# Kernel tuning notes

Hardware: AMD Instinct MI355X
Metric: run time of the kernel (lower is better)

## Reference

```python
import jax, jax.numpy as jnp
import numpy as np

MIN_SIZE = 16.0 / 800.0
PRE_NMS_TOP_K = 6000   # mode='test'
POST_NMS_TOP_K = 300   # mode='test'
IOU_THR = 0.7
H = W = 100
A = 9
N = H * W * A


def setup_inputs() -> dict:
    key = jax.random.key(0)
    k1, k2, k3 = jax.random.split(key, 3)
    pred_cls = jax.random.normal(k1, (1, H, W, 2 * A), dtype=jnp.float32)
    pred_reg = jax.random.normal(k2, (1, N, 4), dtype=jnp.float32) * 0.2
    # anchors as valid normalized xyxy boxes
    u = jax.random.uniform(k3, (N, 4), dtype=jnp.float32)
    cx = 0.05 + 0.9 * u[:, 0]
    cy = 0.05 + 0.9 * u[:, 1]
    w = 0.02 + 0.18 * u[:, 2]
    h = 0.02 + 0.18 * u[:, 3]
    anchor = jnp.stack([cx - w / 2, cy - h / 2, cx + w / 2, cy + h / 2], axis=1)
    return {"pred_cls": pred_cls, "pred_reg": pred_reg, "anchor": anchor}


def greedy_nms_mask(boxes, valid):
    # boxes: [K,4] sorted by descending score; valid: [K] bool
    K = boxes.shape[0]
    area = (boxes[:, 2] - boxes[:, 0]) * (boxes[:, 3] - boxes[:, 1])
    lt = jnp.maximum(boxes[:, None, :2], boxes[None, :, :2])   # [K,K,2]
    rb = jnp.minimum(boxes[:, None, 2:], boxes[None, :, 2:])
    wh = jnp.clip(rb - lt, 0.0)
    inter = wh[..., 0] * wh[..., 1]
    union = area[:, None] + area[None, :] - inter
    iou = inter / jnp.maximum(union, jnp.float32(1e-12))       # [K,K]
    idx = jnp.arange(K)

    def body(i, suppressed):
        keep_i = jnp.logical_not(suppressed[i]) & valid[i]
        return suppressed | (keep_i & (iou[i] > IOU_THR) & (idx > i))

    suppressed = jax.lax.fori_loop(0, K, body, jnp.zeros((K,), dtype=bool))
    return jnp.logical_not(suppressed) & valid


def reference(pred_cls, pred_reg, anchor):
    reg = pred_reg.reshape(-1, 4)                 # squeeze -> [N,4]
    # xy_to_cxcy(anchor)
    a_cxcy = jnp.concatenate([(anchor[:, 2:] + anchor[:, :2]) / 2,
                              anchor[:, 2:] - anchor[:, :2]], axis=1)
    # decode(reg, anchor_cxcy)
    cxcy = reg[:, :2] * a_cxcy[:, 2:] + a_cxcy[:, :2]
    wh = jnp.exp(reg[:, 2:]) * a_cxcy[:, 2:]
    # cxcy_to_xy(...).clamp(0,1)
    roi = jnp.clip(jnp.concatenate([cxcy - wh / 2, cxcy + wh / 2], axis=1), 0.0, 1.0)

    # objectness softmax over the 2-class logits
    probs = jax.nn.softmax(pred_cls.reshape(1, H, W, A, 2), axis=-1)[..., 1].reshape(-1)  # [N]

    # size filter
    ws = roi[:, 2] - roi[:, 0]
    hs = roi[:, 3] - roi[:, 1]
    size_ok = (hs >= MIN_SIZE) & (ws >= MIN_SIZE)
    masked_scores = jnp.where(size_ok, probs, -jnp.inf)

    # sort descending + take pre-NMS top-k (filtered boxes sort last)
    top_scores, top_idx = jax.lax.top_k(masked_scores, PRE_NMS_TOP_K)
    boxes = roi[top_idx]                           # [K,4]
    valid = size_ok[top_idx]

    kept = greedy_nms_mask(boxes, valid)           # [K] bool

    # first POST_NMS_TOP_K kept boxes in score order; pad with zeros
    rank = jnp.cumsum(kept.astype(jnp.int32)) - 1
    slot = jnp.where(kept & (rank < POST_NMS_TOP_K), rank, POST_NMS_TOP_K)
    out = jnp.zeros((POST_NMS_TOP_K, 4), dtype=boxes.dtype).at[slot].set(boxes, mode='drop')
    return out
```

## Files before the change

### kernel.cpp

```cpp
#include <hip/hip_runtime.h>
#include <stdint.h>

#pragma clang fp contract(off)

#define N_ANCH 90000
#define M_TOP  1024
#define M_L    512
#define NW_L   8
#define K_POST 300
#define CAP    2048
#define WINB   0x3D00
#define WINSZ  768
#define DB     32
#define MIN_SIZE (16.0f / 800.0f)
#define IOU_THR  0.7f

#define SIDX(j) ((j) + ((j) >> 6))
#define SB_SZ   (M_L + NW_L)

#define OFF_HISTB 0
#define OFF_CNT   98304
#define OFF_CAND  98368
#define OFF_ROI   114752
#define OFF_KEYS  1554752
#define OFF_SBOX  1914752
#define OFF_MASK  1931136

__global__ void __launch_bounds__(1024)
decode_score_kernel(const float2* __restrict__ cls,
                    const float4* __restrict__ reg,
                    const float4* __restrict__ anc,
                    float4* __restrict__ roi,
                    unsigned* __restrict__ keys,
                    int* __restrict__ histB) {
    __shared__ int lh[WINSZ];
    int tid = threadIdx.x;
    for (int k = tid; k < WINSZ; k += 1024) lh[k] = 0;
    __syncthreads();

    for (int n = blockIdx.x * 1024 + tid; n < N_ANCH; n += DB * 1024) {
        float4 a = anc[n];
        float4 r = reg[n];
        float aw  = a.z - a.x;
        float ah  = a.w - a.y;
        float acx = (a.z + a.x) * 0.5f;
        float acy = (a.w + a.y) * 0.5f;
        float cx = r.x * aw + acx;
        float cy = r.y * ah + acy;
        float w  = expf(r.z) * aw;
        float h  = expf(r.w) * ah;
        float x1 = fminf(fmaxf(cx - w * 0.5f, 0.0f), 1.0f);
        float y1 = fminf(fmaxf(cy - h * 0.5f, 0.0f), 1.0f);
        float x2 = fminf(fmaxf(cx + w * 0.5f, 0.0f), 1.0f);
        float y2 = fminf(fmaxf(cy + h * 0.5f, 0.0f), 1.0f);
        roi[n] = make_float4(x1, y1, x2, y2);

        float2 c = cls[n];
        float m  = fmaxf(c.x, c.y);
        float e0 = expf(c.x - m);
        float e1 = expf(c.y - m);
        float p  = e1 / (e0 + e1);

        bool ok = ((x2 - x1) >= MIN_SIZE) && ((y2 - y1) >= MIN_SIZE);
        unsigned key = ok ? (__float_as_uint(p) ^ 0x80000000u) : 0u;
        keys[n] = key;
        if (key != 0u) {
            int hb = (int)(key >> 16) - 0x8000;
            if (hb >= WINB) atomicAdd(&lh[hb - WINB], 1);
        }
    }
    __syncthreads();
    for (int k = tid; k < WINSZ; k += 1024)
        histB[blockIdx.x * WINSZ + k] = lh[k];
}

__global__ void __launch_bounds__(1024)
thrcompact_kernel(const unsigned* __restrict__ keys,
                  const int* __restrict__ histB,
                  int* __restrict__ cnt,
                  unsigned long long* __restrict__ cand) {
    __shared__ int rscan[1024];
    __shared__ int s_pos;
    __shared__ unsigned s_thr;
    int t = threadIdx.x;
    if (t == 0) s_pos = 0;
    int wsum = 0;
    if (t < WINSZ) {
        int bin = WINSZ - 1 - t;
#pragma unroll
        for (int b = 0; b < DB; ++b) wsum += histB[b * WINSZ + bin];
    }
    rscan[t] = wsum;
    __syncthreads();
    for (int off = 1; off < 1024; off <<= 1) {
        int add = (t >= off) ? rscan[t - off] : 0;
        __syncthreads();
        rscan[t] += add;
        __syncthreads();
    }
    if (t < WINSZ && rscan[t] >= M_TOP && (t == 0 || rscan[t - 1] < M_TOP))
        s_thr = ((unsigned)(0x8000 + WINB + (WINSZ - 1 - t))) << 16;
    if (t == 0 && rscan[WINSZ - 1] < M_TOP)
        s_thr = 0x80000000u;
    __syncthreads();
    unsigned thr = s_thr;
    const uint4* k4 = (const uint4*)keys;
    for (int g = t; g < N_ANCH / 4; g += 1024) {
        uint4 kv = k4[g];
        int n0 = g * 4;
        if (kv.x >= thr) { int p = atomicAdd(&s_pos, 1); if (p < CAP) cand[p] = ((unsigned long long)kv.x << 32) | (unsigned)(~(unsigned)n0); }
        if (kv.y >= thr) { int p = atomicAdd(&s_pos, 1); if (p < CAP) cand[p] = ((unsigned long long)kv.y << 32) | (unsigned)(~(unsigned)(n0 + 1)); }
        if (kv.z >= thr) { int p = atomicAdd(&s_pos, 1); if (p < CAP) cand[p] = ((unsigned long long)kv.z << 32) | (unsigned)(~(unsigned)(n0 + 2)); }
        if (kv.w >= thr) { int p = atomicAdd(&s_pos, 1); if (p < CAP) cand[p] = ((unsigned long long)kv.w << 32) | (unsigned)(~(unsigned)(n0 + 3)); }
    }
    __syncthreads();
    if (t == 0) cnt[0] = (s_pos < CAP) ? s_pos : CAP;
}

__global__ void __launch_bounds__(1024)
rank_select_kernel(const unsigned long long* __restrict__ cand,
                   const int* __restrict__ cnt,
                   const float4* __restrict__ roi,
                   float4* __restrict__ sbox) {
    __shared__ unsigned long long s[CAP];
    __shared__ int red[1024];
    int tid = threadIdx.x;
    int c = cnt[0];
    if (c > CAP) c = CAP;
    for (int k = tid; k < CAP; k += 1024) s[k] = (k < c) ? cand[k] : 0ULL;
    __syncthreads();
    int e = tid & 63;
    int slice = tid >> 6;
    int i = blockIdx.x * 64 + e;
    unsigned long long v = (i < c) ? s[i] : 0ULL;
    int cnt_gt = 0;
    if (i < c) {
        int kbeg = slice * (CAP / 16);
        int kend = kbeg + (CAP / 16);
        if (kend > c) kend = c;
#pragma unroll 4
        for (int k = kbeg; k < kend; ++k)
            cnt_gt += (s[k] > v) ? 1 : 0;
    }
    red[tid] = cnt_gt;
    __syncthreads();
    if (slice == 0 && i < c) {
        int rank = 0;
#pragma unroll
        for (int q = 0; q < 16; ++q) rank += red[e + 64 * q];
        if (rank < M_TOP) {
            unsigned idx = ~((unsigned)v);
            sbox[rank] = roi[idx];
        }
    }
}

__global__ void __launch_bounds__(256)
mask_kernel(const float4* __restrict__ sbox,
            unsigned long long* __restrict__ mask) {
    __shared__ float4 sb[SB_SZ];
    int tid = threadIdx.x;
#pragma unroll
    for (int q = 0; q < M_L / 256; ++q) {
        int j = tid + q * 256;
        sb[SIDX(j)] = sbox[j];
    }
    __syncthreads();
    int wid = blockIdx.x * 256 + tid;
    int i = wid >> 3;
    int w = wid & 7;
    unsigned long long bits = 0;
    int j0 = w << 6;
    if (j0 + 63 > i) {
        float4 bi = sb[SIDX(i)];
        float ai = (bi.z - bi.x) * (bi.w - bi.y);
        for (int b = 0; b < 64; ++b) {
            int j = j0 + b;
            if (j > i) {
                float4 bj = sb[SIDX(j)];
                float xx1 = fmaxf(bi.x, bj.x);
                float yy1 = fmaxf(bi.y, bj.y);
                float xx2 = fminf(bi.z, bj.z);
                float yy2 = fminf(bi.w, bj.w);
                float ww = fmaxf(xx2 - xx1, 0.0f);
                float hh = fmaxf(yy2 - yy1, 0.0f);
                float inter = ww * hh;
                float aj = (bj.z - bj.x) * (bj.w - bj.y);
                float uni = ai + aj - inter;
                float iou = inter / fmaxf(uni, 1e-12f);
                if (iou > IOU_THR) bits |= 1ull << b;
            }
        }
    }
    mask[wid] = bits;
}

__device__ __forceinline__ unsigned long long readlane64(unsigned long long v, int sl) {
    unsigned lo = (unsigned)__builtin_amdgcn_readlane((int)(unsigned)v, sl);
    unsigned hi = (unsigned)__builtin_amdgcn_readlane((int)(unsigned)(v >> 32), sl);
    return ((unsigned long long)hi << 32) | lo;
}

__global__ void __launch_bounds__(64)
walk_kernel(const unsigned long long* __restrict__ mask,
            const float4* __restrict__ sbox,
            const int* __restrict__ cnt,
            float4* __restrict__ out) {
    __shared__ int s_keep[K_POST];
    __shared__ int s_kc;
    int lane = threadIdx.x;
    int c_eff = cnt[0];
    if (c_eff > M_TOP) c_eff = M_TOP;

    unsigned long long diag[NW_L];
#pragma unroll
    for (int cc = 0; cc < NW_L; ++cc)
        diag[cc] = mask[(((cc << 6) | lane) << 3) + cc];

    unsigned long long remw = 0;
    int w = lane & 7;
    int kgrp = lane >> 3;
    int kc = 0;
    bool stop = false;
#pragma unroll
    for (int cc = 0; cc < NW_L; ++cc) {
        int base = cc << 6;
        unsigned long long valid =
            (c_eff >= base + 64) ? ~0ull
          : ((c_eff <= base) ? 0ull : ((1ull << (c_eff - base)) - 1ull));
        unsigned long long live = valid & ~readlane64(remw, cc);
        unsigned long long keptbits = 0;
        while (live) {
            int b = __ffsll((unsigned long long)live) - 1;
            keptbits |= 1ull << b;
            if (lane == 0) s_keep[kc] = base + b;
            ++kc;
            if (kc >= K_POST) { stop = true; break; }
            live &= ~readlane64(diag[cc], b);
            live &= ~(1ull << b);
        }
        if (stop) break;
        if (cc == NW_L - 1) break;
        if (keptbits) {
            int nk = __popcll(keptbits);
            int mypos = 0;
            if (lane < nk) {
                unsigned long long tmp = keptbits;
                for (int p = 0; p < lane; ++p) tmp &= tmp - 1;
                mypos = base + (__ffsll((unsigned long long)tmp) - 1);
            }
            unsigned long long acc = 0;
#pragma unroll
            for (int r = 0; r < 8; ++r) {
                int kg = (r << 3) | kgrp;
                int row = __shfl(mypos, kg);
                unsigned long long v = (kg < nk) ? mask[(row << 3) + w] : 0ull;
                acc |= v;
            }
            acc |= __shfl_xor(acc, 8);
            acc |= __shfl_xor(acc, 16);
            acc |= __shfl_xor(acc, 32);
            remw |= acc;
        }
    }
    if (!stop) {
        for (int i = M_L; i < c_eff && kc < K_POST; ++i) {
            float4 bi = sbox[i];
            float ai = (bi.z - bi.x) * (bi.w - bi.y);
            bool any = false;
            for (int k = lane; k < kc; k += 64) {
                float4 bk = sbox[s_keep[k]];
                float xx1 = fmaxf(bi.x, bk.x);
                float yy1 = fmaxf(bi.y, bk.y);
                float xx2 = fminf(bi.z, bk.z);
                float yy2 = fminf(bi.w, bk.w);
                float ww = fmaxf(xx2 - xx1, 0.0f);
                float hh = fmaxf(yy2 - yy1, 0.0f);
                float inter = ww * hh;
                float ak = (bk.z - bk.x) * (bk.w - bk.y);
                float uni = ai + ak - inter;
                if (inter / fmaxf(uni, 1e-12f) > IOU_THR) any = true;
            }
            if (__ballot(any) == 0ull) {
                if (lane == 0) s_keep[kc] = i;
                ++kc;
            }
        }
    }
    if (lane == 0) s_kc = kc;
    __syncthreads();
    int kcf = s_kc;
    for (int j = lane; j < K_POST; j += 64)
        out[j] = (j < kcf) ? sbox[s_keep[j]] : make_float4(0.f, 0.f, 0.f, 0.f);
}

extern "C" void kernel_launch(void* const* d_in, const int* in_sizes, int n_in,
                              void* d_out, int out_size, void* d_ws, size_t ws_size,
                              hipStream_t stream) {
    const float2* cls = (const float2*)d_in[0];
    const float4* reg = (const float4*)d_in[1];
    const float4* anc = (const float4*)d_in[2];
    float4* out = (float4*)d_out;

    char* ws = (char*)d_ws;
    int*       histB = (int*)(ws + OFF_HISTB);
    int*       cnt   = (int*)(ws + OFF_CNT);
    unsigned long long* cand = (unsigned long long*)(ws + OFF_CAND);
    float4*    roi   = (float4*)(ws + OFF_ROI);
    unsigned*  keys  = (unsigned*)(ws + OFF_KEYS);
    float4*    sbox  = (float4*)(ws + OFF_SBOX);
    unsigned long long* mask = (unsigned long long*)(ws + OFF_MASK);

    decode_score_kernel<<<DB, 1024, 0, stream>>>(cls, reg, anc, roi, keys, histB);
    thrcompact_kernel<<<1, 1024, 0, stream>>>(keys, histB, cnt, cand);
    rank_select_kernel<<<CAP / 64, 1024, 0, stream>>>(cand, cnt, roi, sbox);
    mask_kernel<<<M_L * NW_L / 256, 256, 0, stream>>>(sbox, mask);
    walk_kernel<<<1, 64, 0, stream>>>(mask, sbox, cnt, out);
}
```

Baseline: 136.7 us.

## Fuse five-kernel NMS pipeline into one cooperative kernel with grid syncs

Replaces the five separate launches (decode/score, threshold compaction, rank select, IoU mask, greedy walk) with a single cooperative kernel of 88 blocks that separates stages with grid.sync. Each thread decodes exactly one anchor and keeps its key in a register, so the keys array is no longer written to or reread from global memory. The per-block histogram is stored as 16-bit values and reduced redundantly by every block. This is meant to remove launch gaps and inter-kernel round trips, at the cost of grid-wide barrier overhead and a smaller grid, and it falls back to the old multi-kernel path if the cooperative launch is unsupported or fails.

Result: slower. 250.7 us (+83.3%).

```diff
diff --git a/kernel.cpp b/kernel.cpp
--- a/kernel.cpp
+++ b/kernel.cpp
@@ -1,5 +1,8 @@
 #include <hip/hip_runtime.h>
+#include <hip/hip_cooperative_groups.h>
 #include <stdint.h>
+
+namespace cg = cooperative_groups;
 
 #pragma clang fp contract(off)
 
@@ -11,13 +14,22 @@
 #define CAP    2048
 #define WINB   0x3D00
 #define WINSZ  768
-#define DB     32
 #define MIN_SIZE (16.0f / 800.0f)
 #define IOU_THR  0.7f
 
+#define NBLK 88
+
 #define SIDX(j) ((j) + ((j) >> 6))
 #define SB_SZ   (M_L + NW_L)
 
+#define COFF_CNT   0
+#define COFF_HIST  64
+#define COFF_CAND  135232
+#define COFF_ROI   151616
+#define COFF_SBOX  1591616
+#define COFF_MASK  1608000
+
+#define DB 32
 #define OFF_HISTB 0
 #define OFF_CNT   98304
 #define OFF_CAND  98368
@@ -25,6 +37,279 @@
 #define OFF_KEYS  1554752
 #define OFF_SBOX  1914752
 #define OFF_MASK  1931136
+
+__device__ __forceinline__ unsigned long long readlane64(unsigned long long v, int sl) {
+    unsigned lo = (unsigned)__builtin_amdgcn_readlane((int)(unsigned)v, sl);
+    unsigned hi = (unsigned)__builtin_amdgcn_readlane((int)(unsigned)(v >> 32), sl);
+    return ((unsigned long long)hi << 32) | lo;
+}
+
+__global__ void __launch_bounds__(1024, 4)
+mega_kernel(const float2* __restrict__ cls,
+            const float4* __restrict__ reg,
+            const float4* __restrict__ anc,
+            float4* __restrict__ out,
+            int* __restrict__ cnt,
+            unsigned short* __restrict__ hist,
+            unsigned long long* __restrict__ cand,
+            float4* __restrict__ roi,
+            float4* __restrict__ sbox,
+            unsigned long long* __restrict__ gmask)
+{
+    cg::grid_group grid = cg::this_grid();
+    const int bid = blockIdx.x;
+    const int tid = threadIdx.x;
+
+    __shared__ int lh[WINSZ];
+    __shared__ int rscan[1024];
+    __shared__ unsigned s_thr;
+    __shared__ int wcnt[16], wpre[16], s_base;
+    __shared__ unsigned long long s_cand[CAP];
+    __shared__ int red[1024];
+    __shared__ float4 sb[SB_SZ];
+    __shared__ int s_keep[K_POST];
+    __shared__ int s_kc;
+
+    if (tid < WINSZ) lh[tid] = 0;
+    if (bid == 0 && tid == 0) cnt[0] = 0;
+    __syncthreads();
+
+    const int n = bid * 1024 + tid;
+    unsigned key = 0u;
+    if (n < N_ANCH) {
+        float4 a = anc[n];
+        float4 r = reg[n];
+        float aw  = a.z - a.x;
+        float ah  = a.w - a.y;
+        float acx = (a.z + a.x) * 0.5f;
+        float acy = (a.w + a.y) * 0.5f;
+        float cx = r.x * aw + acx;
+        float cy = r.y * ah + acy;
+        float w  = expf(r.z) * aw;
+        float h  = expf(r.w) * ah;
+        float x1 = fminf(fmaxf(cx - w * 0.5f, 0.0f), 1.0f);
+        float y1 = fminf(fmaxf(cy - h * 0.5f, 0.0f), 1.0f);
+        float x2 = fminf(fmaxf(cx + w * 0.5f, 0.0f), 1.0f);
+        float y2 = fminf(fmaxf(cy + h * 0.5f, 0.0f), 1.0f);
+        roi[n] = make_float4(x1, y1, x2, y2);
+
+        float2 c = cls[n];
+        float m  = fmaxf(c.x, c.y);
+        float e0 = expf(c.x - m);
+        float e1 = expf(c.y - m);
+        float p  = e1 / (e0 + e1);
+
+        bool ok = ((x2 - x1) >= MIN_SIZE) && ((y2 - y1) >= MIN_SIZE);
+        key = ok ? (__float_as_uint(p) ^ 0x80000000u) : 0u;
+        if (key != 0u) {
+            int hb = (int)(key >> 16) - 0x8000;
+            if (hb >= WINB) atomicAdd(&lh[hb - WINB], 1);
+        }
+    }
+    __syncthreads();
+    if (tid < WINSZ) hist[bid * WINSZ + tid] = (unsigned short)lh[tid];
+    __threadfence();
+    grid.sync();
+
+    int wsum = 0;
+    if (tid < WINSZ) {
+        const int bin = WINSZ - 1 - tid;
+        const unsigned short* hp = hist + bin;
+#pragma unroll 8
+        for (int b = 0; b < NBLK; ++b) wsum += (int)hp[b * WINSZ];
+    }
+    rscan[tid] = wsum;
+    __syncthreads();
+    for (int off = 1; off < 1024; off <<= 1) {
+        int add = (tid >= off) ? rscan[tid - off] : 0;
+        __syncthreads();
+        rscan[tid] += add;
+        __syncthreads();
+    }
+    if (tid < WINSZ && rscan[tid] >= M_TOP && (tid == 0 || rscan[tid - 1] < M_TOP))
+        s_thr = ((unsigned)(0x8000 + WINB + (WINSZ - 1 - tid))) << 16;
+    if (tid == 0 && rscan[WINSZ - 1] < M_TOP)
+        s_thr = 0x80000000u;
+    __syncthreads();
+    const unsigned thr = s_thr;
+
+    bool pass = (key >= thr);
+    unsigned long long bal = __ballot(pass);
+    const int wv = tid >> 6, ln = tid & 63;
+    if (ln == 0) wcnt[wv] = __popcll(bal);
+    __syncthreads();
+    if (tid == 0) {
+        int s = 0;
+#pragma unroll
+        for (int q = 0; q < 16; ++q) { wpre[q] = s; s += wcnt[q]; }
+        s_base = s ? atomicAdd(cnt, s) : 0;
+    }
+    __syncthreads();
+    if (pass) {
+        int pos = s_base + wpre[wv] + __popcll(bal & ((1ull << ln) - 1ull));
+        if (pos < CAP) cand[pos] = ((unsigned long long)key << 32) | (unsigned)(~(unsigned)n);
+    }
+    __threadfence();
+    grid.sync();
+
+    if (bid < CAP / 64) {
+        int c = cnt[0];
+        if (c > CAP) c = CAP;
+        for (int k = tid; k < CAP; k += 1024) s_cand[k] = (k < c) ? cand[k] : 0ULL;
+        __syncthreads();
+        int e = tid & 63;
+        int slice = tid >> 6;
+        int i = bid * 64 + e;
+        unsigned long long v = (i < c) ? s_cand[i] : 0ULL;
+        int cnt_gt = 0;
+        if (i < c) {
+            int kbeg = slice * (CAP / 16);
+            int kend = kbeg + (CAP / 16);
+            if (kend > c) kend = c;
+#pragma unroll 4
+            for (int k = kbeg; k < kend; ++k)
+                cnt_gt += (s_cand[k] > v) ? 1 : 0;
+        }
+        red[tid] = cnt_gt;
+        __syncthreads();
+        if (slice == 0 && i < c) {
+            int rank = 0;
+#pragma unroll
+            for (int q = 0; q < 16; ++q) rank += red[e + 64 * q];
+            if (rank < M_TOP) {
+                unsigned idx = ~((unsigned)v);
+                sbox[rank] = roi[idx];
+            }
+        }
+    }
+    __threadfence();
+    grid.sync();
+
+    if (bid < 16) {
+        for (int j = tid; j < M_L; j += 1024) sb[SIDX(j)] = sbox[j];
+        __syncthreads();
+        if (tid < 256) {
+            int wid = bid * 256 + tid;
+            int i = wid >> 3;
+            int w = wid & 7;
+            unsigned long long bits = 0;
+            int j0 = w << 6;
+            if (j0 + 63 > i) {
+                float4 bi = sb[SIDX(i)];
+                float ai = (bi.z - bi.x) * (bi.w - bi.y);
+                for (int b = 0; b < 64; ++b) {
+                    int j = j0 + b;
+                    if (j > i) {
+                        float4 bj = sb[SIDX(j)];
+                        float xx1 = fmaxf(bi.x, bj.x);
+                        float yy1 = fmaxf(bi.y, bj.y);
+                        float xx2 = fminf(bi.z, bj.z);
+                        float yy2 = fminf(bi.w, bj.w);
+                        float ww = fmaxf(xx2 - xx1, 0.0f);
+                        float hh = fmaxf(yy2 - yy1, 0.0f);
+                        float inter = ww * hh;
+                        float aj = (bj.z - bj.x) * (bj.w - bj.y);
+                        float uni = ai + aj - inter;
+                        float iou = inter / fmaxf(uni, 1e-12f);
+                        if (iou > IOU_THR) bits |= 1ull << b;
+                    }
+                }
+            }
+            gmask[wid] = bits;
+        }
+    }
+    __threadfence();
+    grid.sync();
+
+    if (bid == 0) {
+        if (tid < 64) {
+            int lane = tid;
+            int c_eff = cnt[0];
+            if (c_eff > M_TOP) c_eff = M_TOP;
+
+            unsigned long long diag[NW_L];
+#pragma unroll
+            for (int cc = 0; cc < NW_L; ++cc)
+                diag[cc] = gmask[(((cc << 6) | lane) << 3) + cc];
+
+            unsigned long long remw = 0;
+            int w = lane & 7;
+            int kgrp = lane >> 3;
+            int kc = 0;
+            bool stop = false;
+#pragma unroll
+            for (int cc = 0; cc < NW_L; ++cc) {
+                int base = cc << 6;
+                unsigned long long valid =
+                    (c_eff >= base + 64) ? ~0ull
+                  : ((c_eff <= base) ? 0ull : ((1ull << (c_eff - base)) - 1ull));
+                unsigned long long live = valid & ~readlane64(remw, cc);
+                unsigned long long keptbits = 0;
+                while (live) {
+                    int b = __ffsll((unsigned long long)live) - 1;
+                    keptbits |= 1ull << b;
+                    if (lane == 0) s_keep[kc] = base + b;
+                    ++kc;
+                    if (kc >= K_POST) { stop = true; break; }
+                    live &= ~readlane64(diag[cc], b);
+                    live &= ~(1ull << b);
+                }
+                if (stop) break;
+                if (cc == NW_L - 1) break;
+                if (keptbits) {
+                    int nk = __popcll(keptbits);
+                    int mypos = 0;
+                    if (lane < nk) {
+                        unsigned long long tmp = keptbits;
+                        for (int p = 0; p < lane; ++p) tmp &= tmp - 1;
+                        mypos = base + (__ffsll((unsigned long long)tmp) - 1);
+                    }
+                    unsigned long long acc = 0;
+#pragma unroll
+                    for (int r = 0; r < 8; ++r) {
+                        int kg = (r << 3) | kgrp;
+                        int row = __shfl(mypos, kg);
+                        unsigned long long v = (kg < nk) ? gmask[(row << 3) + w] : 0ull;
+                        acc |= v;
+                    }
+                    acc |= __shfl_xor(acc, 8);
+                    acc |= __shfl_xor(acc, 16);
+                    acc |= __shfl_xor(acc, 32);
+                    remw |= acc;
+                }
+            }
+            if (!stop) {
+                for (int i = M_L; i < c_eff && kc < K_POST; ++i) {
+                    float4 bi = sbox[i];
+                    float ai = (bi.z - bi.x) * (bi.w - bi.y);
+                    bool any = false;
+                    for (int k = lane; k < kc; k += 64) {
+                        float4 bk = sbox[s_keep[k]];
+                        float xx1 = fmaxf(bi.x, bk.x);
+                        float yy1 = fmaxf(bi.y, bk.y);
+                        float xx2 = fminf(bi.z, bk.z);
+                        float yy2 = fminf(bi.w, bk.w);
+                        float ww = fmaxf(xx2 - xx1, 0.0f);
+                        float hh = fmaxf(yy2 - yy1, 0.0f);
+                        float inter = ww * hh;
+                        float ak = (bk.z - bk.x) * (bk.w - bk.y);
+                        float uni = ai + ak - inter;
+                        if (inter / fmaxf(uni, 1e-12f) > IOU_THR) any = true;
+                    }
+                    if (__ballot(any) == 0ull) {
+                        if (lane == 0) s_keep[kc] = i;
+                        ++kc;
+                    }
+                }
+            }
+            if (lane == 0) s_kc = kc;
+        }
+        __syncthreads();
+        int kcf = s_kc;
+        for (int j = tid; j < K_POST; j += 1024)
+            out[j] = (j < kcf) ? sbox[s_keep[j]] : make_float4(0.f, 0.f, 0.f, 0.f);
+    }
+}
 
 __global__ void __launch_bounds__(1024)
 decode_score_kernel(const float2* __restrict__ cls,
@@ -37,7 +322,6 @@
     int tid = threadIdx.x;
     for (int k = tid; k < WINSZ; k += 1024) lh[k] = 0;
     __syncthreads();
-
     for (int n = blockIdx.x * 1024 + tid; n < N_ANCH; n += DB * 1024) {
         float4 a = anc[n];
         float4 r = reg[n];
@@ -54,13 +338,11 @@
         float x2 = fminf(fmaxf(cx + w * 0.5f, 0.0f), 1.0f);
         float y2 = fminf(fmaxf(cy + h * 0.5f, 0.0f), 1.0f);
         roi[n] = make_float4(x1, y1, x2, y2);
-
         float2 c = cls[n];
         float m  = fmaxf(c.x, c.y);
         float e0 = expf(c.x - m);
         float e1 = expf(c.y - m);
         float p  = e1 / (e0 + e1);
-
         bool ok = ((x2 - x1) >= MIN_SIZE) && ((y2 - y1) >= MIN_SIZE);
         unsigned key = ok ? (__float_as_uint(p) ^ 0x80000000u) : 0u;
         keys[n] = key;
@@ -195,12 +477,6 @@
     mask[wid] = bits;
 }
 
-__device__ __forceinline__ unsigned long long readlane64(unsigned long long v, int sl) {
-    unsigned lo = (unsigned)__builtin_amdgcn_readlane((int)(unsigned)v, sl);
-    unsigned hi = (unsigned)__builtin_amdgcn_readlane((int)(unsigned)(v >> 32), sl);
-    return ((unsigned long long)hi << 32) | lo;
-}
-
 __global__ void __launch_bounds__(64)
 walk_kernel(const unsigned long long* __restrict__ mask,
             const float4* __restrict__ sbox,
@@ -211,12 +487,10 @@
     int lane = threadIdx.x;
     int c_eff = cnt[0];
     if (c_eff > M_TOP) c_eff = M_TOP;
-
     unsigned long long diag[NW_L];
 #pragma unroll
     for (int cc = 0; cc < NW_L; ++cc)
         diag[cc] = mask[(((cc << 6) | lane) << 3) + cc];
-
     unsigned long long remw = 0;
     int w = lane & 7;
     int kgrp = lane >> 3;
@@ -301,8 +575,33 @@
     const float4* reg = (const float4*)d_in[1];
     const float4* anc = (const float4*)d_in[2];
     float4* out = (float4*)d_out;
-
     char* ws = (char*)d_ws;
+
+    static int coop = -1;
+    if (coop < 0) {
+        int dev = 0, v = 0;
+        hipGetDevice(&dev);
+        hipDeviceGetAttribute(&v, hipDeviceAttributeCooperativeLaunch, dev);
+        coop = v;
+    }
+    if (coop) {
+        int* cnt = (int*)(ws + COFF_CNT);
+        unsigned short* hist = (unsigned short*)(ws + COFF_HIST);
+        unsigned long long* cand = (unsigned long long*)(ws + COFF_CAND);
+        float4* roi  = (float4*)(ws + COFF_ROI);
+        float4* sbox = (float4*)(ws + COFF_SBOX);
+        unsigned long long* gmask = (unsigned long long*)(ws + COFF_MASK);
+        void* args[] = { (void*)&cls, (void*)&reg, (void*)&anc, (void*)&out,
+                         (void*)&cnt, (void*)&hist, (void*)&cand, (void*)&roi,
+                         (void*)&sbox, (void*)&gmask };
+        hipError_t e = hipLaunchCooperativeKernel((const void*)mega_kernel,
+                                                  dim3(NBLK), dim3(1024),
+                                                  args, 0, stream);
+        if (e == hipSuccess) return;
+        (void)hipGetLastError();
+        coop = 0;
+    }
+
     int*       histB = (int*)(ws + OFF_HISTB);
     int*       cnt   = (int*)(ws + OFF_CNT);
     unsigned long long* cand = (unsigned long long*)(ws + OFF_CAND);
```

## Parallelize decode and compaction across blocks, stage NMS mask in LDS

Applied to the files above, without the earlier changes.

Decode now runs one anchor per thread over 88 blocks and writes a transposed 16-bit per-block histogram. Compaction is split across 32 blocks, which use wave ballots and a single global atomic per block instead of per-element shared atomics. The walk kernel first copies the whole suppression mask into shared memory so the serial walk reads LDS instead of global memory. Workspace regions are overlapped to save space. Candidate order now depends on which block wins the atomic, and the later rank step must absorb that nondeterminism.

After: 123.1 us. -9.9%, faster.

```diff
diff --git a/kernel.cpp b/kernel.cpp
--- a/kernel.cpp
+++ b/kernel.cpp
@@ -11,34 +11,41 @@
 #define CAP    2048
 #define WINB   0x3D00
 #define WINSZ  768
-#define DB     32
 #define MIN_SIZE (16.0f / 800.0f)
 #define IOU_THR  0.7f
 
+#define NB_D 88
+#define NB_C 32
+#define GPB  704
+
 #define SIDX(j) ((j) + ((j) >> 6))
 #define SB_SZ   (M_L + NW_L)
 
-#define OFF_HISTB 0
-#define OFF_CNT   98304
-#define OFF_CAND  98368
-#define OFF_ROI   114752
-#define OFF_KEYS  1554752
-#define OFF_SBOX  1914752
-#define OFF_MASK  1931136
+#define OFF_CNT   0
+#define OFF_HIST  64
+#define OFF_MASK  64
+#define OFF_CAND  135232
+#define OFF_ROI   151616
+#define OFF_KEYS  1591616
+#define OFF_SBOX  1591616
 
 __global__ void __launch_bounds__(1024)
-decode_score_kernel(const float2* __restrict__ cls,
-                    const float4* __restrict__ reg,
-                    const float4* __restrict__ anc,
-                    float4* __restrict__ roi,
-                    unsigned* __restrict__ keys,
-                    int* __restrict__ histB) {
+decode_kernel(const float2* __restrict__ cls,
+              const float4* __restrict__ reg,
+              const float4* __restrict__ anc,
+              float4* __restrict__ roi,
+              unsigned* __restrict__ keys,
+              unsigned short* __restrict__ hist,
+              int* __restrict__ cnt) {
     __shared__ int lh[WINSZ];
-    int tid = threadIdx.x;
-    for (int k = tid; k < WINSZ; k += 1024) lh[k] = 0;
-    __syncthreads();
-
-    for (int n = blockIdx.x * 1024 + tid; n < N_ANCH; n += DB * 1024) {
+    const int tid = threadIdx.x;
+    const int bid = blockIdx.x;
+    if (tid < WINSZ) lh[tid] = 0;
+    if (bid == 0 && tid == 0) cnt[0] = 0;
+    __syncthreads();
+
+    const int n = bid * 1024 + tid;
+    if (n < N_ANCH) {
         float4 a = anc[n];
         float4 r = reg[n];
         float aw  = a.z - a.x;
@@ -70,25 +77,30 @@
         }
     }
     __syncthreads();
-    for (int k = tid; k < WINSZ; k += 1024)
-        histB[blockIdx.x * WINSZ + k] = lh[k];
+    if (tid < WINSZ) hist[tid * NB_D + bid] = (unsigned short)lh[tid];
 }
 
 __global__ void __launch_bounds__(1024)
-thrcompact_kernel(const unsigned* __restrict__ keys,
-                  const int* __restrict__ histB,
-                  int* __restrict__ cnt,
-                  unsigned long long* __restrict__ cand) {
+compact_kernel(const unsigned* __restrict__ keys,
+               const unsigned short* __restrict__ hist,
+               int* __restrict__ cnt,
+               unsigned long long* __restrict__ cand) {
     __shared__ int rscan[1024];
-    __shared__ int s_pos;
     __shared__ unsigned s_thr;
-    int t = threadIdx.x;
-    if (t == 0) s_pos = 0;
+    __shared__ int wcnt[16], wbase[16];
+    __shared__ int s_base;
+    const int t = threadIdx.x;
+
     int wsum = 0;
     if (t < WINSZ) {
-        int bin = WINSZ - 1 - t;
-#pragma unroll
-        for (int b = 0; b < DB; ++b) wsum += histB[b * WINSZ + bin];
+        const int bin = WINSZ - 1 - t;
+        const uint4* hp = (const uint4*)(hist + bin * NB_D);
+#pragma unroll
+        for (int q = 0; q < 11; ++q) {
+            uint4 v = hp[q];
+            wsum += (int)((v.x & 0xffffu) + (v.x >> 16) + (v.y & 0xffffu) + (v.y >> 16)
+                        + (v.z & 0xffffu) + (v.z >> 16) + (v.w & 0xffffu) + (v.w >> 16));
+        }
     }
     rscan[t] = wsum;
     __syncthreads();
@@ -103,18 +115,44 @@
     if (t == 0 && rscan[WINSZ - 1] < M_TOP)
         s_thr = 0x80000000u;
     __syncthreads();
-    unsigned thr = s_thr;
+    const unsigned thr = s_thr;
+
     const uint4* k4 = (const uint4*)keys;
-    for (int g = t; g < N_ANCH / 4; g += 1024) {
-        uint4 kv = k4[g];
+    const int g = blockIdx.x * GPB + t;
+    const int gend0 = (blockIdx.x + 1) * GPB;
+    const int gend = (gend0 < N_ANCH / 4) ? gend0 : (N_ANCH / 4);
+    unsigned pm = 0;
+    uint4 kv = make_uint4(0u, 0u, 0u, 0u);
+    if (t < GPB && g < gend) {
+        kv = k4[g];
+        pm = (kv.x >= thr ? 1u : 0u) | (kv.y >= thr ? 2u : 0u)
+           | (kv.z >= thr ? 4u : 0u) | (kv.w >= thr ? 8u : 0u);
+    }
+    unsigned long long b0 = __ballot((pm & 1u) != 0u);
+    unsigned long long b1 = __ballot((pm & 2u) != 0u);
+    unsigned long long b2 = __ballot((pm & 4u) != 0u);
+    unsigned long long b3 = __ballot((pm & 8u) != 0u);
+    const int ln = t & 63, wv = t >> 6;
+    if (ln == 0)
+        wcnt[wv] = __popcll(b0) + __popcll(b1) + __popcll(b2) + __popcll(b3);
+    __syncthreads();
+    if (t == 0) {
+        int s = 0;
+#pragma unroll
+        for (int q = 0; q < 16; ++q) { wbase[q] = s; s += wcnt[q]; }
+        s_base = s ? atomicAdd(cnt, s) : 0;
+    }
+    __syncthreads();
+    if (pm) {
+        unsigned long long lt = (ln == 0) ? 0ull : ((1ull << ln) - 1ull);
+        int pos = s_base + wbase[wv]
+                + __popcll(b0 & lt) + __popcll(b1 & lt) + __popcll(b2 & lt) + __popcll(b3 & lt);
         int n0 = g * 4;
-        if (kv.x >= thr) { int p = atomicAdd(&s_pos, 1); if (p < CAP) cand[p] = ((unsigned long long)kv.x << 32) | (unsigned)(~(unsigned)n0); }
-        if (kv.y >= thr) { int p = atomicAdd(&s_pos, 1); if (p < CAP) cand[p] = ((unsigned long long)kv.y << 32) | (unsigned)(~(unsigned)(n0 + 1)); }
-        if (kv.z >= thr) { int p = atomicAdd(&s_pos, 1); if (p < CAP) cand[p] = ((unsigned long long)kv.z << 32) | (unsigned)(~(unsigned)(n0 + 2)); }
-        if (kv.w >= thr) { int p = atomicAdd(&s_pos, 1); if (p < CAP) cand[p] = ((unsigned long long)kv.w << 32) | (unsigned)(~(unsigned)(n0 + 3)); }
-    }
-    __syncthreads();
-    if (t == 0) cnt[0] = (s_pos < CAP) ? s_pos : CAP;
+        if (pm & 1u) { if (pos < CAP) cand[pos] = ((unsigned long long)kv.x << 32) | (unsigned)(~(unsigned)n0);       ++pos; }
+        if (pm & 2u) { if (pos < CAP) cand[pos] = ((unsigned long long)kv.y << 32) | (unsigned)(~(unsigned)(n0 + 1)); ++pos; }
+        if (pm & 4u) { if (pos < CAP) cand[pos] = ((unsigned long long)kv.z << 32) | (unsigned)(~(unsigned)(n0 + 2)); ++pos; }
+        if (pm & 8u) { if (pos < CAP) cand[pos] = ((unsigned long long)kv.w << 32) | (unsigned)(~(unsigned)(n0 + 3)); ++pos; }
+    }
 }
 
 __global__ void __launch_bounds__(1024)
@@ -201,96 +239,110 @@
     return ((unsigned long long)hi << 32) | lo;
 }
 
-__global__ void __launch_bounds__(64)
+__global__ void __launch_bounds__(256)
 walk_kernel(const unsigned long long* __restrict__ mask,
             const float4* __restrict__ sbox,
             const int* __restrict__ cnt,
             float4* __restrict__ out) {
+    __shared__ unsigned long long lmask[M_L * NW_L];
     __shared__ int s_keep[K_POST];
     __shared__ int s_kc;
-    int lane = threadIdx.x;
-    int c_eff = cnt[0];
-    if (c_eff > M_TOP) c_eff = M_TOP;
-
-    unsigned long long diag[NW_L];
-#pragma unroll
-    for (int cc = 0; cc < NW_L; ++cc)
-        diag[cc] = mask[(((cc << 6) | lane) << 3) + cc];
-
-    unsigned long long remw = 0;
-    int w = lane & 7;
-    int kgrp = lane >> 3;
-    int kc = 0;
-    bool stop = false;
-#pragma unroll
-    for (int cc = 0; cc < NW_L; ++cc) {
-        int base = cc << 6;
-        unsigned long long valid =
-            (c_eff >= base + 64) ? ~0ull
-          : ((c_eff <= base) ? 0ull : ((1ull << (c_eff - base)) - 1ull));
-        unsigned long long live = valid & ~readlane64(remw, cc);
-        unsigned long long keptbits = 0;
-        while (live) {
-            int b = __ffsll((unsigned long long)live) - 1;
-            keptbits |= 1ull << b;
-            if (lane == 0) s_keep[kc] = base + b;
-            ++kc;
-            if (kc >= K_POST) { stop = true; break; }
-            live &= ~readlane64(diag[cc], b);
-            live &= ~(1ull << b);
-        }
-        if (stop) break;
-        if (cc == NW_L - 1) break;
-        if (keptbits) {
-            int nk = __popcll(keptbits);
-            int mypos = 0;
-            if (lane < nk) {
-                unsigned long long tmp = keptbits;
-                for (int p = 0; p < lane; ++p) tmp &= tmp - 1;
-                mypos = base + (__ffsll((unsigned long long)tmp) - 1);
+    const int tid = threadIdx.x;
+
+    {
+        const uint4* src = (const uint4*)mask;
+        uint4* dst = (uint4*)lmask;
+#pragma unroll
+        for (int q = 0; q < (M_L * NW_L) / 2 / 256; ++q)
+            dst[tid + q * 256] = src[tid + q * 256];
+    }
+    __syncthreads();
+
+    if (tid < 64) {
+        int lane = tid;
+        int c_eff = cnt[0];
+        if (c_eff > M_TOP) c_eff = M_TOP;
+
+        unsigned long long diag[NW_L];
+#pragma unroll
+        for (int cc = 0; cc < NW_L; ++cc)
+            diag[cc] = lmask[(((cc << 6) | lane) << 3) + cc];
+
+        unsigned long long remw = 0;
+        int w = lane & 7;
+        int kgrp = lane >> 3;
+        int kc = 0;
+        bool stop = false;
+#pragma unroll
+        for (int cc = 0; cc < NW_L; ++cc) {
+            int base = cc << 6;
+            unsigned long long valid =
+                (c_eff >= base + 64) ? ~0ull
+              : ((c_eff <= base) ? 0ull : ((1ull << (c_eff - base)) - 1ull));
+            unsigned long long live = valid & ~readlane64(remw, cc);
+            unsigned long long keptbits = 0;
+            while (live) {
+                int b = __ffsll((unsigned long long)live) - 1;
+                keptbits |= 1ull << b;
+                if (lane == 0) s_keep[kc] = base + b;
+                ++kc;
+                if (kc >= K_POST) { stop = true; break; }
+                live &= ~readlane64(diag[cc], b);
+                live &= ~(1ull << b);
             }
-            unsigned long long acc = 0;
-#pragma unroll
-            for (int r = 0; r < 8; ++r) {
-                int kg = (r << 3) | kgrp;
-                int row = __shfl(mypos, kg);
-                unsigned long long v = (kg < nk) ? mask[(row << 3) + w] : 0ull;
-                acc |= v;
+            if (stop) break;
+            if (cc == NW_L - 1) break;
+            if (keptbits) {
+                int nk = __popcll(keptbits);
+                int mypos = 0;
+                if (lane < nk) {
+                    unsigned long long tmp = keptbits;
+                    for (int p = 0; p < lane; ++p) tmp &= tmp - 1;
+                    mypos = base + (__ffsll((unsigned long long)tmp) - 1);
+                }
+                unsigned long long acc = 0;
+#pragma unroll
+                for (int r = 0; r < 8; ++r) {
+                    int kg = (r << 3) | kgrp;
+                    int row = __shfl(mypos, kg);
+                    unsigned long long v = (kg < nk) ? lmask[(row << 3) + w] : 0ull;
+                    acc |= v;
+                }
+                acc |= __shfl_xor(acc, 8);
+                acc |= __shfl_xor(acc, 16);
+                acc |= __shfl_xor(acc, 32);
+                remw |= acc;
             }
-            acc |= __shfl_xor(acc, 8);
-            acc |= __shfl_xor(acc, 16);
-            acc |= __shfl_xor(acc, 32);
-            remw |= acc;
-        }
-    }
-    if (!stop) {
-        for (int i = M_L; i < c_eff && kc < K_POST; ++i) {
-            float4 bi = sbox[i];
-            float ai = (bi.z - bi.x) * (bi.w - bi.y);
-            bool any = false;
-            for (int k = lane; k < kc; k += 64) {
-                float4 bk = sbox[s_keep[k]];
-                float xx1 = fmaxf(bi.x, bk.x);
-                float yy1 = fmaxf(bi.y, bk.y);
-                float xx2 = fminf(bi.z, bk.z);
-                float yy2 = fminf(bi.w, bk.w);
-                float ww = fmaxf(xx2 - xx1, 0.0f);
-                float hh = fmaxf(yy2 - yy1, 0.0f);
-                float inter = ww * hh;
-                float ak = (bk.z - bk.x) * (bk.w - bk.y);
-                float uni = ai + ak - inter;
-                if (inter / fmaxf(uni, 1e-12f) > IOU_THR) any = true;
+        }
+        if (!stop) {
+            for (int i = M_L; i < c_eff && kc < K_POST; ++i) {
+                float4 bi = sbox[i];
+                float ai = (bi.z - bi.x) * (bi.w - bi.y);
+                bool any = false;
+                for (int k = lane; k < kc; k += 64) {
+                    float4 bk = sbox[s_keep[k]];
+                    float xx1 = fmaxf(bi.x, bk.x);
+                    float yy1 = fmaxf(bi.y, bk.y);
+                    float xx2 = fminf(bi.z, bk.z);
+                    float yy2 = fminf(bi.w, bk.w);
+                    float ww = fmaxf(xx2 - xx1, 0.0f);
+                    float hh = fmaxf(yy2 - yy1, 0.0f);
+                    float inter = ww * hh;
+                    float ak = (bk.z - bk.x) * (bk.w - bk.y);
+                    float uni = ai + ak - inter;
+                    if (inter / fmaxf(uni, 1e-12f) > IOU_THR) any = true;
+                }
+                if (__ballot(any) == 0ull) {
+                    if (lane == 0) s_keep[kc] = i;
+                    ++kc;
+                }
             }
-            if (__ballot(any) == 0ull) {
-                if (lane == 0) s_keep[kc] = i;
-                ++kc;
-            }
-        }
-    }
-    if (lane == 0) s_kc = kc;
+        }
+        if (lane == 0) s_kc = kc;
+    }
     __syncthreads();
     int kcf = s_kc;
-    for (int j = lane; j < K_POST; j += 64)
+    for (int j = tid; j < K_POST; j += 256)
         out[j] = (j < kcf) ? sbox[s_keep[j]] : make_float4(0.f, 0.f, 0.f, 0.f);
 }
 
@@ -303,17 +355,17 @@
     float4* out = (float4*)d_out;
 
     char* ws = (char*)d_ws;
-    int*       histB = (int*)(ws + OFF_HISTB);
-    int*       cnt   = (int*)(ws + OFF_CNT);
+    int*                cnt  = (int*)(ws + OFF_CNT);
+    unsigned short*     hist = (unsigned short*)(ws + OFF_HIST);
+    unsigned long long* mask = (unsigned long long*)(ws + OFF_MASK);
     unsigned long long* cand = (unsigned long long*)(ws + OFF_CAND);
-    float4*    roi   = (float4*)(ws + OFF_ROI);
-    unsigned*  keys  = (unsigned*)(ws + OFF_KEYS);
-    float4*    sbox  = (float4*)(ws + OFF_SBOX);
-    unsigned long long* mask = (unsigned long long*)(ws + OFF_MASK);
-
-    decode_score_kernel<<<DB, 1024, 0, stream>>>(cls, reg, anc, roi, keys, histB);
-    thrcompact_kernel<<<1, 1024, 0, stream>>>(keys, histB, cnt, cand);
+    float4*             roi  = (float4*)(ws + OFF_ROI);
+    unsigned*           keys = (unsigned*)(ws + OFF_KEYS);
+    float4*             sbox = (float4*)(ws + OFF_SBOX);
+
+    decode_kernel<<<NB_D, 1024, 0, stream>>>(cls, reg, anc, roi, keys, hist, cnt);
+    compact_kernel<<<NB_C, 1024, 0, stream>>>(keys, hist, cnt, cand);
     rank_select_kernel<<<CAP / 64, 1024, 0, stream>>>(cand, cnt, roi, sbox);
     mask_kernel<<<M_L * NW_L / 256, 256, 0, stream>>>(sbox, mask);
-    walk_kernel<<<1, 64, 0, stream>>>(mask, sbox, cnt, out);
-}
+    walk_kernel<<<1, 256, 0, stream>>>(mask, sbox, cnt, out);
+}
```
